# Kernel tuning notes

Measured on AMD Instinct MI355X. Metric: run time of the kernel, lower is better.

The kernel has to match this reference:

```python
import jax, jax.numpy as jnp
import numpy as np

B, L, D, H, DFF = 4, 2048, 1024, 16, 4096
DH = D // H
INF = 1e12


def setup_inputs() -> dict:
    key = jax.random.key(0)
    ks = jax.random.split(key, 20)
    s = lambda fan_in: 1.0 / np.sqrt(fan_in)
    inp = {
        'x': jax.random.normal(ks[0], (B, L, D), jnp.float32),
        'mask': jax.random.bernoulli(ks[1], 0.1, (B, 1, 1, L)),
        'wq': jax.random.normal(ks[2], (D, D), jnp.float32) * s(D),
        'bq': jnp.zeros((D,), jnp.float32),
        'wk': jax.random.normal(ks[3], (D, D), jnp.float32) * s(D),
        'bk': jnp.zeros((D,), jnp.float32),
        'wv': jax.random.normal(ks[4], (D, D), jnp.float32) * s(D),
        'bv': jnp.zeros((D,), jnp.float32),
        'wo': jax.random.normal(ks[5], (D, D), jnp.float32) * s(D),
        'bo': jnp.zeros((D,), jnp.float32),
        'w1': jax.random.normal(ks[6], (D, DFF), jnp.float32) * s(D),
        'b1': jnp.zeros((DFF,), jnp.float32),
        'w2': jax.random.normal(ks[7], (DFF, D), jnp.float32) * s(DFF),
        'b2': jnp.zeros((D,), jnp.float32),
        'g1': jnp.ones((D,), jnp.float32),
        'beta1': jnp.zeros((D,), jnp.float32),
        'g2': jnp.ones((D,), jnp.float32),
        'beta2': jnp.zeros((D,), jnp.float32),
    }
    return inp


def _layernorm(x, g, b, eps=1e-5):
    mu = jnp.mean(x, axis=-1, keepdims=True)
    var = jnp.mean(jnp.square(x - mu), axis=-1, keepdims=True)
    return (x - mu) * jax.lax.rsqrt(var + eps) * g + b


def reference(x, mask, wq, bq, wk, bk, wv, bv, wo, bo, w1, b1, w2, b2, g1, beta1, g2, beta2):
    # --- self attention ---
    def split_heads(t):  # [B,L,D] -> [B,H,L,DH]
        return t.reshape(B, L, H, DH).transpose(0, 2, 1, 3)

    Q = split_heads(x @ wq + bq)
    K = split_heads(x @ wk + bk)
    V = split_heads(x @ wv + bv)

    dots = jnp.einsum('bhqd,bhkd->bhqk', Q, K) / np.sqrt(DH)  # [B,H,L,L]
    dots = jnp.where(mask, -INF, dots)
    attn = jax.nn.softmax(dots, axis=-1)
    out = jnp.einsum('bhqk,bhkd->bhqd', attn, V)
    out = out.transpose(0, 2, 1, 3).reshape(B, L, D)
    out = out @ wo + bo

    x = _layernorm(x + out, g1, beta1)

    # --- feed forward ---
    h = jax.nn.relu(x @ w1 + b1)
    ff = h @ w2 + b2
    x = _layernorm(x + ff, g2, beta2)
    return x
```

## Files before the change

kernel.cpp:

```cpp
#include <hip/hip_runtime.h>
#include <hip/hip_bf16.h>

#define B_   4
#define L_   2048
#define D_   1024
#define H_   16
#define DH_  64
#define DFF_ 4096
#define M_   (B_ * L_)

typedef __attribute__((ext_vector_type(8))) short bf16x8;
typedef __attribute__((ext_vector_type(4))) float f32x4;

#define GLOAD16(gp, lp)                                                       \
  __builtin_amdgcn_global_load_lds(                                           \
      (const __attribute__((address_space(1))) unsigned int*)(gp),            \
      (__attribute__((address_space(3))) unsigned int*)(lp), 16, 0, 0)

#if __has_builtin(__builtin_amdgcn_exp2f)
#define EXP2F(x) __builtin_amdgcn_exp2f(x)
#else
#define EXP2F(x) exp2f(x)
#endif

__device__ __forceinline__ float bf2f(unsigned short u) {
  return __uint_as_float(((unsigned)u) << 16);
}

__global__ void prep_all(const float4* __restrict__ x4,
                         ushort4* __restrict__ xb4,
                         const unsigned int* __restrict__ mraw,
                         float* __restrict__ maskf,
                         const float* __restrict__ bq,
                         const float* __restrict__ bk,
                         const float* __restrict__ bv,
                         float* __restrict__ biasc) {
  const int id = blockIdx.x;
  if (id < 8192) {
    const int i = id * 256 + threadIdx.x;
    float4 v = x4[i];
    __hip_bfloat16 a = __float2bfloat16(v.x);
    __hip_bfloat16 b = __float2bfloat16(v.y);
    __hip_bfloat16 c = __float2bfloat16(v.z);
    __hip_bfloat16 d = __float2bfloat16(v.w);
    ushort4 o;
    o.x = *reinterpret_cast<unsigned short*>(&a);
    o.y = *reinterpret_cast<unsigned short*>(&b);
    o.z = *reinterpret_cast<unsigned short*>(&c);
    o.w = *reinterpret_cast<unsigned short*>(&d);
    xb4[i] = o;
    return;
  }
  __shared__ int flags[2];
  if (threadIdx.x < 2) flags[threadIdx.x] = 0;
  __syncthreads();
  int nf32 = 0, n01 = 0;
  for (int i = threadIdx.x; i < 2048; i += 256) {
    unsigned w = mraw[i];
    if (w != 0u && w != 0x3f800000u) nf32 = 1;
    if (w > 1u) n01 = 1;
  }
  if (nf32) atomicOr(&flags[0], 1);
  if (n01)  atomicOr(&flags[1], 1);
  __syncthreads();
  const int mode = (!flags[0]) ? 0 : ((!flags[1]) ? 1 : 2);
  const int mi = (id - 8192) * 256 + threadIdx.x;
  if (mi < B_ * L_) {
    bool mk;
    if (mode == 0)      mk = reinterpret_cast<const float*>(mraw)[mi] != 0.f;
    else if (mode == 1) mk = reinterpret_cast<const int*>(mraw)[mi] != 0;
    else                mk = reinterpret_cast<const unsigned char*>(mraw)[mi] != 0;
    maskf[mi] = mk ? -1e12f : -32.0f;
  }
  if (id == 8192) {
#pragma unroll
    for (int j = 0; j < 4; ++j) {
      const int c = j * 256 + threadIdx.x;
      biasc[c] = bq[c];
      biasc[D_ + c] = bk[c];
      biasc[2 * D_ + c] = bv[c];
    }
  }
}

__global__ void transpose_cvt_all(
    const float* __restrict__ wq, const float* __restrict__ wk,
    const float* __restrict__ wv, const float* __restrict__ wo,
    const float* __restrict__ w1, const float* __restrict__ w2,
    __hip_bfloat16* __restrict__ WQT, __hip_bfloat16* __restrict__ WKT,
    __hip_bfloat16* __restrict__ WVT, __hip_bfloat16* __restrict__ WOT,
    __hip_bfloat16* __restrict__ W1T, __hip_bfloat16* __restrict__ W2T) {
  __shared__ float t[32][33];
  const int id = blockIdx.x;
  const float* W;
  __hip_bfloat16* Wt;
  int K, N, rem;
  if (id < 4096) {
    const int which = id >> 10;
    W  = which == 0 ? wq : which == 1 ? wk : which == 2 ? wv : wo;
    Wt = which == 0 ? WQT : which == 1 ? WKT : which == 2 ? WVT : WOT;
    K = D_; N = D_; rem = id & 1023;
  } else if (id < 8192) {
    W = w1; Wt = W1T; K = D_; N = DFF_; rem = id - 4096;
  } else {
    W = w2; Wt = W2T; K = DFF_; N = D_; rem = id - 8192;
  }
  const int ntx = N >> 5;
  const int n0 = (rem % ntx) * 32, k0 = (rem / ntx) * 32;
  const int tx = threadIdx.x, ty = threadIdx.y;
#pragma unroll
  for (int i = 0; i < 4; ++i)
    t[ty + i * 8][tx] = W[(size_t)(k0 + ty + i * 8) * N + n0 + tx];
  __syncthreads();
#pragma unroll
  for (int i = 0; i < 4; ++i)
    Wt[(size_t)(n0 + ty + i * 8) * K + k0 + tx] =
        __float2bfloat16(t[tx][ty + i * 8]);
}

__global__ void transpose_v(const __hip_bfloat16* __restrict__ Vin,
                            __hip_bfloat16* __restrict__ Vt) {
  __shared__ __hip_bfloat16 t[32][33];
  const int l0 = blockIdx.x * 32, d0 = blockIdx.y * 32, b = blockIdx.z;
  const int tx = threadIdx.x, ty = threadIdx.y;
#pragma unroll
  for (int i = 0; i < 4; ++i)
    t[ty + i * 8][tx] = Vin[(size_t)(b * L_ + l0 + ty + i * 8) * D_ + d0 + tx];
  __syncthreads();
#pragma unroll
  for (int i = 0; i < 4; ++i) {
    int d = d0 + ty + i * 8;
    Vt[(size_t)(b * D_ + d) * L_ + l0 + tx] = t[tx][ty + i * 8];
  }
}

#define STAGE8(matptr, stride, ldsbase, tile, kh, rowbase)                    \
  {                                                                           \
    _Pragma("unroll")                                                         \
    for (int j_ = 0; j_ < 2; ++j_) {                                          \
      const int s_ = j_ * 512 + tid;                                          \
      const int row_ = s_ >> 2;                                               \
      const int q_ = (s_ & 3) ^ ((row_ >> 1) & 3);                            \
      GLOAD16(&matptr[(size_t)((rowbase) + row_) * (stride) + (tile) * 64 +   \
                      (kh) * 32 + q_ * 8],                                    \
              (ldsbase) + (j_ * 512 + (w << 6)) * 16);                        \
    }                                                                         \
  }

#define PHASE8(bufoff, rh, ks, dovm, ...)                                     \
  {                                                                           \
    if ((rh) == 0) {                                                          \
      _Pragma("unroll")                                                       \
      for (int j = 0; j < 4; ++j) {                                           \
        const int br = wn * 64 + j * 16 + r16;                                \
        bfr[j] = *reinterpret_cast<const bf16x8*>(                            \
            ldsB + (bufoff) + (ks) * 16384 + br * 64 +                        \
            ((hi * 16) ^ (((br >> 1) & 3) << 4)));                            \
      }                                                                       \
    }                                                                         \
    bf16x8 af[4];                                                             \
    _Pragma("unroll")                                                         \
    for (int i = 0; i < 4; ++i) {                                             \
      const int ar = wm * 128 + (rh) * 64 + i * 16 + r16;                     \
      af[i] = *reinterpret_cast<const bf16x8*>(                               \
          ldsA + (bufoff) + (ks) * 16384 + ar * 64 +                          \
          ((hi * 16) ^ (((ar >> 1) & 3) << 4)));                              \
    }                                                                         \
    __VA_ARGS__;                                                              \
    __builtin_amdgcn_s_barrier();                                             \
    asm volatile("s_waitcnt lgkmcnt(0)" ::: "memory");                        \
    __builtin_amdgcn_sched_barrier(0);                                        \
    __builtin_amdgcn_s_setprio(1);                                            \
    _Pragma("unroll")                                                         \
    for (int i = 0; i < 4; ++i)                                               \
      _Pragma("unroll")                                                       \
      for (int j = 0; j < 4; ++j)                                             \
        acc[(rh) * 4 + i][j] = __builtin_amdgcn_mfma_f32_16x16x32_bf16(       \
            af[i], bfr[j], acc[(rh) * 4 + i][j], 0, 0, 0);                    \
    __builtin_amdgcn_s_setprio(0);                                            \
    if (dovm) {                                                               \
      asm volatile("s_waitcnt vmcnt(4)" ::: "memory");                        \
      __builtin_amdgcn_sched_barrier(0);                                      \
    }                                                                         \
    __builtin_amdgcn_s_barrier();                                             \
  }

template <int EP>
__global__ __launch_bounds__(512, 1) void gemm8(
    const __hip_bfloat16* __restrict__ A, const __hip_bfloat16* __restrict__ Bt,
    const float* __restrict__ bias, void* __restrict__ out,
    int M, int N, int K, int lda, int ldb) {
  __shared__ __align__(16) char lds8[131072];
  char* const ldsA = lds8;
  char* const ldsB = lds8 + 65536;

  const int tid = threadIdx.x;
  const int lane = tid & 63;
  const int w = tid >> 6;
  const int wm = w >> 2;
  const int wn = w & 3;
  const int r16 = lane & 15;
  const int hi = lane >> 4;

  const int nwg = gridDim.x;
  const int orig = blockIdx.x;
  const int swz = (orig & 7) * (nwg >> 3) + (orig >> 3);

  int bm, bn, kh = 0;
  const __hip_bfloat16* Ap = A;
  const __hip_bfloat16* Bp = Bt;
  if (EP == 4) {
    kh = swz & 1;
    const int rest = swz >> 1;
    bm = (rest & 31) * 256;
    bn = (rest >> 5) * 256;
    Ap += (size_t)kh * K;
    Bp += (size_t)kh * K;
  } else {
    bm = (swz & 31) * 256;
    bn = (swz >> 5) * 256;
  }

  f32x4 acc[8][4];
#pragma unroll
  for (int i = 0; i < 8; ++i)
#pragma unroll
    for (int j = 0; j < 4; ++j) acc[i][j] = (f32x4){0.f, 0.f, 0.f, 0.f};
  bf16x8 bfr[4];

  const int nkt = K >> 6;
  const int nit = nkt >> 1;

  STAGE8(Ap, lda, ldsA, 0, 0, bm);
  STAGE8(Bp, ldb, ldsB, 0, 0, bn);
  STAGE8(Ap, lda, ldsA + 16384, 0, 1, bm);
  STAGE8(Bp, ldb, ldsB + 16384, 0, 1, bn);
  STAGE8(Ap, lda, ldsA + 32768, 1, 0, bm);
  STAGE8(Bp, ldb, ldsB + 32768, 1, 0, bn);
  asm volatile("s_waitcnt vmcnt(4)" ::: "memory");
  __builtin_amdgcn_sched_barrier(0);
  __builtin_amdgcn_s_barrier();

  for (int it = 0; it < nit; ++it) {
    const int kt = it * 2;
    const bool hn = (it + 1) < nit;
    PHASE8(0, 0, 0, 0, STAGE8(Ap, lda, ldsA + 49152, kt + 1, 1, bm));
    PHASE8(0, 1, 0, 0, STAGE8(Bp, ldb, ldsB + 49152, kt + 1, 1, bn));
    PHASE8(0, 0, 1, 0, if (hn) STAGE8(Ap, lda, ldsA, kt + 2, 0, bm));
    PHASE8(0, 1, 1, 1, if (hn) STAGE8(Bp, ldb, ldsB, kt + 2, 0, bn));
    PHASE8(32768, 0, 0, 0, if (hn) STAGE8(Ap, lda, ldsA + 16384, kt + 2, 1, bm));
    PHASE8(32768, 1, 0, 0, if (hn) STAGE8(Bp, ldb, ldsB + 16384, kt + 2, 1, bn));
    PHASE8(32768, 0, 1, 0, if (hn) STAGE8(Ap, lda, ldsA + 32768, kt + 3, 0, bm));
    PHASE8(32768, 1, 1, 1, if (hn) STAGE8(Bp, ldb, ldsB + 32768, kt + 3, 0, bn));
  }

#pragma unroll
  for (int ri = 0; ri < 8; ++ri) {
#pragma unroll
    for (int j = 0; j < 4; ++j) {
      const int col = bn + wn * 64 + j * 16 + r16;
      const float bv = (EP == 4) ? 0.f : bias[col];
#pragma unroll
      for (int r = 0; r < 4; ++r) {
        const int row = bm + wm * 128 + ri * 16 + hi * 4 + r;
        const float v = acc[ri][j][r] + bv;
        if (EP == 1) {
          ((__hip_bfloat16*)out)[(size_t)row * N + col] =
              __float2bfloat16(v > 0.f ? v : 0.f);
        } else if (EP == 3) {
          __hip_bfloat16* outp =
              (__hip_bfloat16*)out + (size_t)(col >> 10) * (M_ * D_);
          outp[(size_t)row * 1024 + (col & 1023)] = __float2bfloat16(v);
        } else {
          __hip_bfloat16* outp =
              (__hip_bfloat16*)out + (size_t)kh * ((size_t)M * N);
          outp[(size_t)row * N + col] = __float2bfloat16(v);
        }
      }
    }
  }
}

template <int EP>
__global__ __launch_bounds__(256) void gemm_bt(
    const __hip_bfloat16* __restrict__ A, const __hip_bfloat16* __restrict__ Bt,
    const float* __restrict__ bias, const float* __restrict__ res,
    void* __restrict__ out, int M, int N, int K) {
  __shared__ __align__(16) char As[128 * 64];
  __shared__ __align__(16) char Bs[128 * 64];
  const int tid = threadIdx.x;
  const int lane = tid & 63;
  const int w = tid >> 6;
  const int wm = w >> 1, wn = w & 1;
  const int bm = blockIdx.x * 128;
  const int bn = blockIdx.y * 128;
  const int r16 = lane & 15;
  const int hi = lane >> 4;

  f32x4 acc[4][4];
#pragma unroll
  for (int m = 0; m < 4; ++m)
#pragma unroll
    for (int n = 0; n < 4; ++n) acc[m][n] = (f32x4){0.f, 0.f, 0.f, 0.f};

  for (int k0 = 0; k0 < K; k0 += 32) {
    __syncthreads();
#pragma unroll
    for (int c = 0; c < 2; ++c) {
      const int seg = c * 256 + tid;
      const int row = seg >> 2;
      const int csl = (seg & 3) ^ (row & 3);
      GLOAD16(&A[(size_t)(bm + row) * K + k0 + csl * 8],
              As + (c * 256 + w * 64) * 16);
      GLOAD16(&Bt[(size_t)(bn + row) * K + k0 + csl * 8],
              Bs + (c * 256 + w * 64) * 16);
    }
    __syncthreads();

    bf16x8 af[4], bfr[4];
#pragma unroll
    for (int m = 0; m < 4; ++m) {
      const int arow = wm * 64 + m * 16 + r16;
      af[m] = *reinterpret_cast<const bf16x8*>(
          As + arow * 64 + ((hi * 16) ^ ((arow & 3) << 4)));
    }
#pragma unroll
    for (int n = 0; n < 4; ++n) {
      const int brow = wn * 64 + n * 16 + r16;
      bfr[n] = *reinterpret_cast<const bf16x8*>(
          Bs + brow * 64 + ((hi * 16) ^ ((brow & 3) << 4)));
    }
#pragma unroll
    for (int m = 0; m < 4; ++m)
#pragma unroll
      for (int n = 0; n < 4; ++n)
        acc[m][n] = __builtin_amdgcn_mfma_f32_16x16x32_bf16(af[m], bfr[n],
                                                            acc[m][n], 0, 0, 0);
  }

  const int rg = hi * 4;
#pragma unroll
  for (int m = 0; m < 4; ++m) {
#pragma unroll
    for (int n = 0; n < 4; ++n) {
      const int col = bn + wn * 64 + n * 16 + r16;
      const float bv = bias[col];
#pragma unroll
      for (int r = 0; r < 4; ++r) {
        const int row = bm + wm * 64 + m * 16 + rg + r;
        const size_t idx = (size_t)row * N + col;
        float v = acc[m][n][r] + bv;
        if (EP == 0) {
          ((__hip_bfloat16*)out)[idx] = __float2bfloat16(v);
        } else {
          ((float*)out)[idx] = v + res[idx];
        }
      }
    }
  }
}

__global__ __launch_bounds__(256) void attn_kernel(
    const __hip_bfloat16* __restrict__ Qg, const __hip_bfloat16* __restrict__ Kg,
    const __hip_bfloat16* __restrict__ VTg,
    const float* __restrict__ maskf,
    __hip_bfloat16* __restrict__ Og) {
  __shared__ __align__(16) char Kl[64 * 128];
  __shared__ __align__(16) char Vl[64 * 128];
  __shared__ __align__(16) char Pl[4][32 * 128];
  __shared__ float maskb[64];

  const int tid = threadIdx.x;
  const int lane = tid & 63;
  const int w = tid >> 6;
  const int hi = lane >> 4;
  const int r16 = lane & 15;
  const int swzk = (r16 & 7) << 4;

  const int nwg = gridDim.x;
  const int orig = blockIdx.x;
  const int swb = (orig & 7) * (nwg >> 3) + (orig >> 3);
  const int qb = swb & 15;
  const int bh = swb >> 4;
  const int b = bh >> 4;
  const int h = bh & 15;
  const int qbase = qb * 128 + w * 32;

  const float C = 0.18033688011112042f;

  bf16x8 qf[2][2];
#pragma unroll
  for (int m = 0; m < 2; ++m)
#pragma unroll
    for (int ks = 0; ks < 2; ++ks)
      qf[m][ks] = *reinterpret_cast<const bf16x8*>(
          &Qg[(size_t)(b * L_ + qbase + m * 16 + r16) * D_ + h * DH_ +
              ks * 32 + hi * 8]);

  float lrun[2] = {0.f, 0.f};
  f32x4 o[2][4];
#pragma unroll
  for (int m = 0; m < 2; ++m)
#pragma unroll
    for (int nd = 0; nd < 4; ++nd) o[m][nd] = (f32x4){0.f, 0.f, 0.f, 0.f};

  char* const Plw = Pl[w];

  for (int kv0 = 0; kv0 < L_; kv0 += 64) {
    __syncthreads();
#pragma unroll
    for (int c = 0; c < 2; ++c) {
      const int seg = c * 256 + tid;
      const int row = seg >> 3;
      const int csl = (seg & 7) ^ (row & 7);
      GLOAD16(&Kg[(size_t)(b * L_ + kv0 + row) * D_ + h * DH_ + csl * 8],
              Kl + (c * 256 + w * 64) * 16);
      GLOAD16(&VTg[(size_t)(b * D_ + h * DH_ + row) * L_ + kv0 + csl * 8],
              Vl + (c * 256 + w * 64) * 16);
    }
    if (tid < 64) maskb[tid] = maskf[(size_t)b * L_ + kv0 + tid];
    __syncthreads();

    f32x4 sacc[2][4];
#pragma unroll
    for (int m = 0; m < 2; ++m)
#pragma unroll
      for (int n = 0; n < 4; ++n) sacc[m][n] = (f32x4){0.f, 0.f, 0.f, 0.f};
    __builtin_amdgcn_s_setprio(1);
#pragma unroll
    for (int n = 0; n < 4; ++n) {
      const int krow = n * 16 + r16;
#pragma unroll
      for (int ks = 0; ks < 2; ++ks) {
        const bf16x8 kf = *reinterpret_cast<const bf16x8*>(
            Kl + krow * 128 + ((ks * 64 + hi * 16) ^ swzk));
#pragma unroll
        for (int m = 0; m < 2; ++m)
          sacc[m][n] = __builtin_amdgcn_mfma_f32_16x16x32_bf16(
              kf, qf[m][ks], sacc[m][n], 0, 0, 0);
      }
    }
    __builtin_amdgcn_s_setprio(0);

#pragma unroll
    for (int m = 0; m < 2; ++m) {
      float ls = 0.f;
      const int prow = m * 16 + r16;
#pragma unroll
      for (int n = 0; n < 4; ++n) {
        const float4 mv =
            *reinterpret_cast<const float4*>(&maskb[n * 16 + hi * 4]);
        const float e0 = EXP2F(fmaf(sacc[m][n][0], C, mv.x));
        const float e1 = EXP2F(fmaf(sacc[m][n][1], C, mv.y));
        const float e2 = EXP2F(fmaf(sacc[m][n][2], C, mv.z));
        const float e3 = EXP2F(fmaf(sacc[m][n][3], C, mv.w));
        ls += (e0 + e1) + (e2 + e3);
        union { unsigned long long u; unsigned short us[4]; } pk;
        __hip_bfloat16 t0 = __float2bfloat16(e0);
        __hip_bfloat16 t1 = __float2bfloat16(e1);
        __hip_bfloat16 t2 = __float2bfloat16(e2);
        __hip_bfloat16 t3 = __float2bfloat16(e3);
        pk.us[0] = *reinterpret_cast<unsigned short*>(&t0);
        pk.us[1] = *reinterpret_cast<unsigned short*>(&t1);
        pk.us[2] = *reinterpret_cast<unsigned short*>(&t2);
        pk.us[3] = *reinterpret_cast<unsigned short*>(&t3);
        *reinterpret_cast<unsigned long long*>(
            Plw + prow * 128 + ((n * 32 + hi * 8) ^ swzk)) = pk.u;
      }
      lrun[m] += ls;
    }

    bf16x8 pa[2][2];
#pragma unroll
    for (int m = 0; m < 2; ++m)
#pragma unroll
      for (int ks = 0; ks < 2; ++ks)
        pa[m][ks] = *reinterpret_cast<const bf16x8*>(
            Plw + (m * 16 + r16) * 128 + ((ks * 64 + hi * 16) ^ swzk));
    __builtin_amdgcn_s_setprio(1);
#pragma unroll
    for (int nd = 0; nd < 4; ++nd) {
      const int vrow = nd * 16 + r16;
#pragma unroll
      for (int ks = 0; ks < 2; ++ks) {
        const bf16x8 vb = *reinterpret_cast<const bf16x8*>(
            Vl + vrow * 128 + ((ks * 64 + hi * 16) ^ swzk));
#pragma unroll
        for (int m = 0; m < 2; ++m)
          o[m][nd] = __builtin_amdgcn_mfma_f32_16x16x32_bf16(pa[m][ks], vb,
                                                             o[m][nd], 0, 0, 0);
      }
    }
    __builtin_amdgcn_s_setprio(0);
  }

#pragma unroll
  for (int m = 0; m < 2; ++m) {
    lrun[m] += __shfl_xor(lrun[m], 16, 64);
    lrun[m] += __shfl_xor(lrun[m], 32, 64);
    const float inv = 1.f / lrun[m];
    float invr[4];
#pragma unroll
    for (int r = 0; r < 4; ++r)
      invr[r] = __shfl(inv, (lane & 48) | (hi * 4 + r), 64);
#pragma unroll
    for (int r = 0; r < 4; ++r) {
      const int q = qbase + m * 16 + hi * 4 + r;
#pragma unroll
      for (int nd = 0; nd < 4; ++nd)
        Og[(size_t)(b * L_ + q) * D_ + h * DH_ + nd * 16 + r16] =
            __float2bfloat16(o[m][nd][r] * invr[r]);
    }
  }
}

__global__ __launch_bounds__(256) void layernorm_kernel(
    const float* __restrict__ in, const float* __restrict__ g,
    const float* __restrict__ be, float* __restrict__ outf,
    __hip_bfloat16* __restrict__ outb) {
  const int row = blockIdx.x;
  const int tid = threadIdx.x;
  const float4 v = reinterpret_cast<const float4*>(in + (size_t)row * D_)[tid];
  float s = v.x + v.y + v.z + v.w;
  float ss = v.x * v.x + v.y * v.y + v.z * v.z + v.w * v.w;
#pragma unroll
  for (int off = 1; off < 64; off <<= 1) {
    s += __shfl_xor(s, off, 64);
    ss += __shfl_xor(ss, off, 64);
  }
  __shared__ float red[8];
  const int w = tid >> 6, lane = tid & 63;
  if (lane == 0) { red[w] = s; red[4 + w] = ss; }
  __syncthreads();
  s = red[0] + red[1] + red[2] + red[3];
  ss = red[4] + red[5] + red[6] + red[7];
  const float mu = s * (1.f / D_);
  const float rs = rsqrtf(ss * (1.f / D_) - mu * mu + 1e-5f);
  const float4 gv = reinterpret_cast<const float4*>(g)[tid];
  const float4 bv = reinterpret_cast<const float4*>(be)[tid];
  float4 ov;
  ov.x = (v.x - mu) * rs * gv.x + bv.x;
  ov.y = (v.y - mu) * rs * gv.y + bv.y;
  ov.z = (v.z - mu) * rs * gv.z + bv.z;
  ov.w = (v.w - mu) * rs * gv.w + bv.w;
  reinterpret_cast<float4*>(outf + (size_t)row * D_)[tid] = ov;
  if (outb) {
    __hip_bfloat16 t[4] = {__float2bfloat16(ov.x), __float2bfloat16(ov.y),
                           __float2bfloat16(ov.z), __float2bfloat16(ov.w)};
    *reinterpret_cast<uint2*>(&outb[(size_t)row * D_ + tid * 4]) =
        *reinterpret_cast<const uint2*>(t);
  }
}

__global__ __launch_bounds__(256) void ln_addres(
    const __hip_bfloat16* __restrict__ OP, const float* __restrict__ x,
    const float* __restrict__ g, const float* __restrict__ be,
    float* __restrict__ outf, __hip_bfloat16* __restrict__ outb) {
  const int row = blockIdx.x;
  const int tid = threadIdx.x;
  const ushort4 a4 = reinterpret_cast<const ushort4*>(OP + (size_t)row * D_)[tid];
  const float4 xr = reinterpret_cast<const float4*>(x + (size_t)row * D_)[tid];
  float4 v;
  v.x = bf2f(a4.x) + xr.x;
  v.y = bf2f(a4.y) + xr.y;
  v.z = bf2f(a4.z) + xr.z;
  v.w = bf2f(a4.w) + xr.w;
  float s = v.x + v.y + v.z + v.w;
  float ss = v.x * v.x + v.y * v.y + v.z * v.z + v.w * v.w;
#pragma unroll
  for (int off = 1; off < 64; off <<= 1) {
    s += __shfl_xor(s, off, 64);
    ss += __shfl_xor(ss, off, 64);
  }
  __shared__ float red[8];
  const int w = tid >> 6, lane = tid & 63;
  if (lane == 0) { red[w] = s; red[4 + w] = ss; }
  __syncthreads();
  s = red[0] + red[1] + red[2] + red[3];
  ss = red[4] + red[5] + red[6] + red[7];
  const float mu = s * (1.f / D_);
  const float rs = rsqrtf(ss * (1.f / D_) - mu * mu + 1e-5f);
  const float4 gv = reinterpret_cast<const float4*>(g)[tid];
  const float4 bv = reinterpret_cast<const float4*>(be)[tid];
  float4 ov;
  ov.x = (v.x - mu) * rs * gv.x + bv.x;
  ov.y = (v.y - mu) * rs * gv.y + bv.y;
  ov.z = (v.z - mu) * rs * gv.z + bv.z;
  ov.w = (v.w - mu) * rs * gv.w + bv.w;
  reinterpret_cast<float4*>(outf + (size_t)row * D_)[tid] = ov;
  __hip_bfloat16 t[4] = {__float2bfloat16(ov.x), __float2bfloat16(ov.y),
                         __float2bfloat16(ov.z), __float2bfloat16(ov.w)};
  *reinterpret_cast<uint2*>(&outb[(size_t)row * D_ + tid * 4]) =
      *reinterpret_cast<const uint2*>(t);
}

__global__ __launch_bounds__(256) void combine_ln2(
    const __hip_bfloat16* __restrict__ P0, const __hip_bfloat16* __restrict__ P1,
    const float* __restrict__ res, const float* __restrict__ b2,
    const float* __restrict__ g, const float* __restrict__ be,
    float* __restrict__ out) {
  const int row = blockIdx.x;
  const int tid = threadIdx.x;
  const ushort4 a4 =
      reinterpret_cast<const ushort4*>(P0 + (size_t)row * D_)[tid];
  const ushort4 b4 =
      reinterpret_cast<const ushort4*>(P1 + (size_t)row * D_)[tid];
  const float4 rr = reinterpret_cast<const float4*>(res + (size_t)row * D_)[tid];
  const float4 bb = reinterpret_cast<const float4*>(b2)[tid];
  float4 v;
  v.x = bf2f(a4.x) + bf2f(b4.x) + rr.x + bb.x;
  v.y = bf2f(a4.y) + bf2f(b4.y) + rr.y + bb.y;
  v.z = bf2f(a4.z) + bf2f(b4.z) + rr.z + bb.z;
  v.w = bf2f(a4.w) + bf2f(b4.w) + rr.w + bb.w;
  float s = v.x + v.y + v.z + v.w;
  float ss = v.x * v.x + v.y * v.y + v.z * v.z + v.w * v.w;
#pragma unroll
  for (int off = 1; off < 64; off <<= 1) {
    s += __shfl_xor(s, off, 64);
    ss += __shfl_xor(ss, off, 64);
  }
  __shared__ float red[8];
  const int w = tid >> 6, lane = tid & 63;
  if (lane == 0) { red[w] = s; red[4 + w] = ss; }
  __syncthreads();
  s = red[0] + red[1] + red[2] + red[3];
  ss = red[4] + red[5] + red[6] + red[7];
  const float mu = s * (1.f / D_);
  const float rs = rsqrtf(ss * (1.f / D_) - mu * mu + 1e-5f);
  const float4 gv = reinterpret_cast<const float4*>(g)[tid];
  const float4 bv = reinterpret_cast<const float4*>(be)[tid];
  float4 ov;
  ov.x = (v.x - mu) * rs * gv.x + bv.x;
  ov.y = (v.y - mu) * rs * gv.y + bv.y;
  ov.z = (v.z - mu) * rs * gv.z + bv.z;
  ov.w = (v.w - mu) * rs * gv.w + bv.w;
  reinterpret_cast<float4*>(out + (size_t)row * D_)[tid] = ov;
}

extern "C" void kernel_launch(void* const* d_in, const int* in_sizes, int n_in,
                              void* d_out, int out_size, void* d_ws,
                              size_t ws_size, hipStream_t stream) {
  (void)in_sizes; (void)n_in; (void)out_size;
  const float* x   = (const float*)d_in[0];
  const void*  msk = d_in[1];
  const float* wq  = (const float*)d_in[2];
  const float* bq  = (const float*)d_in[3];
  const float* wk  = (const float*)d_in[4];
  const float* bk  = (const float*)d_in[5];
  const float* wv  = (const float*)d_in[6];
  const float* bv  = (const float*)d_in[7];
  const float* wo  = (const float*)d_in[8];
  const float* bo  = (const float*)d_in[9];
  const float* w1  = (const float*)d_in[10];
  const float* b1  = (const float*)d_in[11];
  const float* w2  = (const float*)d_in[12];
  const float* b2  = (const float*)d_in[13];
  const float* g1  = (const float*)d_in[14];
  const float* be1 = (const float*)d_in[15];
  const float* g2  = (const float*)d_in[16];
  const float* be2 = (const float*)d_in[17];

  char* ws = (char*)d_ws;
  float*          MASKF = (float*)(ws + 256);
  float*          BIASC = (float*)(ws + 40960);
  __hip_bfloat16* XB    = (__hip_bfloat16*)(ws + 65536);
  __hip_bfloat16* WQT   = (__hip_bfloat16*)(ws + 16842752);
  __hip_bfloat16* WKT   = (__hip_bfloat16*)(ws + 18939904);
  __hip_bfloat16* WVT   = (__hip_bfloat16*)(ws + 21037056);
  __hip_bfloat16* WOT   = (__hip_bfloat16*)(ws + 23134208);
  __hip_bfloat16* W1T   = (__hip_bfloat16*)(ws + 25231360);
  __hip_bfloat16* W2T   = (__hip_bfloat16*)(ws + 33619968);
  __hip_bfloat16* QB    = (__hip_bfloat16*)(ws + 42008576);
  __hip_bfloat16* KB    = (__hip_bfloat16*)(ws + 58785792);
  __hip_bfloat16* VB    = (__hip_bfloat16*)(ws + 75563008);
  __hip_bfloat16* OB    = (__hip_bfloat16*)(ws + 92340224);
  __hip_bfloat16* HB    = QB;
  __hip_bfloat16* VT    = (__hip_bfloat16*)(ws + 109117440);
  __hip_bfloat16* OP    = VT;
  float*          R1    = (float*)(ws + 125894656);
  __hip_bfloat16* P0    = (__hip_bfloat16*)(ws + 159449088);
  __hip_bfloat16* P1    = (__hip_bfloat16*)(ws + 176226304);
  float*          OUT   = (float*)d_out;
  const bool use_splitk = ws_size >= 193003520ull;

  prep_all<<<8224, 256, 0, stream>>>((const float4*)x, (ushort4*)XB,
                                     (const unsigned int*)msk, MASKF,
                                     bq, bk, bv, BIASC);
  transpose_cvt_all<<<12288, dim3(32, 8), 0, stream>>>(
      wq, wk, wv, wo, w1, w2, WQT, WKT, WVT, WOT, W1T, W2T);

  gemm8<3><<<dim3((M_ / 256) * (3 * D_ / 256)), 512, 0, stream>>>(
      XB, WQT, BIASC, QB, M_, 3 * D_, D_, D_, D_);

  transpose_v<<<dim3(L_ / 32, D_ / 32, B_), dim3(32, 8), 0, stream>>>(VB, VT);
  attn_kernel<<<dim3(B_ * H_ * (L_ / 128)), 256, 0, stream>>>(QB, KB, VT, MASKF, OB);

  gemm_bt<0><<<dim3(M_ / 128, D_ / 128), 256, 0, stream>>>(OB, WOT, bo, nullptr, OP, M_, D_, D_);
  ln_addres<<<M_, 256, 0, stream>>>(OP, x, g1, be1, R1, XB);

  gemm8<1><<<dim3((M_ / 256) * (DFF_ / 256)), 512, 0, stream>>>(
      XB, W1T, b1, HB, M_, DFF_, D_, D_, D_);
  if (use_splitk) {
    gemm8<4><<<dim3((M_ / 256) * (D_ / 256) * 2), 512, 0, stream>>>(
        HB, W2T, nullptr, P0, M_, D_, DFF_ / 2, DFF_, DFF_);
    combine_ln2<<<M_, 256, 0, stream>>>(P0, P1, R1, b2, g2, be2, OUT);
  } else {
    gemm_bt<2><<<dim3(M_ / 128, D_ / 128), 256, 0, stream>>>(HB, W2T, b2, R1, OUT, M_, D_, DFF_);
    layernorm_kernel<<<M_, 256, 0, stream>>>(OUT, g2, be2, OUT, nullptr);
  }
}
```

Measured before the change: 433.3 us.

## Compute softmax denominator via MFMA and use split-K gemm8 for output projection

In attention, the per-row sum of exponentials is now taken with an extra MFMA against a ones vector, using the same bf16-rounded probabilities as the PV product. This replaces scalar adds and the cross-lane shuffles at the end. The mask values are loaded once per KV tile instead of once per m iteration. The output projection also switches from gemm_bt to the 256-tile gemm8 split-K path, and the two partials plus bias are combined inside a new fused residual+layernorm kernel. This costs extra MFMA work and bf16 partial traffic, and the denominator is now built from rounded values.

After: 416.8 us. 1.04x faster.

```diff
diff --git a/kernel.cpp b/kernel.cpp
--- a/kernel.cpp
+++ b/kernel.cpp
@@ -387,6 +387,8 @@
   const int qbase = qb * 128 + w * 32;
 
   const float C = 0.18033688011112042f;
+  const short ob = (short)0x3f80;
+  const bf16x8 vone = {ob, ob, ob, ob, ob, ob, ob, ob};
 
   bf16x8 qf[2][2];
 #pragma unroll
@@ -397,12 +399,14 @@
           &Qg[(size_t)(b * L_ + qbase + m * 16 + r16) * D_ + h * DH_ +
               ks * 32 + hi * 8]);
 
-  float lrun[2] = {0.f, 0.f};
   f32x4 o[2][4];
-#pragma unroll
-  for (int m = 0; m < 2; ++m)
+  f32x4 oden[2];
+#pragma unroll
+  for (int m = 0; m < 2; ++m) {
+    oden[m] = (f32x4){0.f, 0.f, 0.f, 0.f};
 #pragma unroll
     for (int nd = 0; nd < 4; ++nd) o[m][nd] = (f32x4){0.f, 0.f, 0.f, 0.f};
+  }
 
   char* const Plw = Pl[w];
 
@@ -442,19 +446,19 @@
     }
     __builtin_amdgcn_s_setprio(0);
 
+    float4 mv[4];
+#pragma unroll
+    for (int n = 0; n < 4; ++n)
+      mv[n] = *reinterpret_cast<const float4*>(&maskb[n * 16 + hi * 4]);
 #pragma unroll
     for (int m = 0; m < 2; ++m) {
-      float ls = 0.f;
       const int prow = m * 16 + r16;
 #pragma unroll
       for (int n = 0; n < 4; ++n) {
-        const float4 mv =
-            *reinterpret_cast<const float4*>(&maskb[n * 16 + hi * 4]);
-        const float e0 = EXP2F(fmaf(sacc[m][n][0], C, mv.x));
-        const float e1 = EXP2F(fmaf(sacc[m][n][1], C, mv.y));
-        const float e2 = EXP2F(fmaf(sacc[m][n][2], C, mv.z));
-        const float e3 = EXP2F(fmaf(sacc[m][n][3], C, mv.w));
-        ls += (e0 + e1) + (e2 + e3);
+        const float e0 = EXP2F(fmaf(sacc[m][n][0], C, mv[n].x));
+        const float e1 = EXP2F(fmaf(sacc[m][n][1], C, mv[n].y));
+        const float e2 = EXP2F(fmaf(sacc[m][n][2], C, mv[n].z));
+        const float e3 = EXP2F(fmaf(sacc[m][n][3], C, mv[n].w));
         union { unsigned long long u; unsigned short us[4]; } pk;
         __hip_bfloat16 t0 = __float2bfloat16(e0);
         __hip_bfloat16 t1 = __float2bfloat16(e1);
@@ -467,7 +471,6 @@
         *reinterpret_cast<unsigned long long*>(
             Plw + prow * 128 + ((n * 32 + hi * 8) ^ swzk)) = pk.u;
       }
-      lrun[m] += ls;
     }
 
     bf16x8 pa[2][2];
@@ -479,6 +482,12 @@
             Plw + (m * 16 + r16) * 128 + ((ks * 64 + hi * 16) ^ swzk));
     __builtin_amdgcn_s_setprio(1);
 #pragma unroll
+    for (int m = 0; m < 2; ++m)
+#pragma unroll
+      for (int ks = 0; ks < 2; ++ks)
+        oden[m] = __builtin_amdgcn_mfma_f32_16x16x32_bf16(pa[m][ks], vone,
+                                                          oden[m], 0, 0, 0);
+#pragma unroll
     for (int nd = 0; nd < 4; ++nd) {
       const int vrow = nd * 16 + r16;
 #pragma unroll
@@ -496,20 +505,14 @@
 
 #pragma unroll
   for (int m = 0; m < 2; ++m) {
-    lrun[m] += __shfl_xor(lrun[m], 16, 64);
-    lrun[m] += __shfl_xor(lrun[m], 32, 64);
-    const float inv = 1.f / lrun[m];
-    float invr[4];
-#pragma unroll
-    for (int r = 0; r < 4; ++r)
-      invr[r] = __shfl(inv, (lane & 48) | (hi * 4 + r), 64);
 #pragma unroll
     for (int r = 0; r < 4; ++r) {
+      const float ir = 1.f / oden[m][r];
       const int q = qbase + m * 16 + hi * 4 + r;
 #pragma unroll
       for (int nd = 0; nd < 4; ++nd)
         Og[(size_t)(b * L_ + q) * D_ + h * DH_ + nd * 16 + r16] =
-            __float2bfloat16(o[m][nd][r] * invr[r]);
+            __float2bfloat16(o[m][nd][r] * ir);
     }
   }
 }
@@ -565,6 +568,51 @@
   v.y = bf2f(a4.y) + xr.y;
   v.z = bf2f(a4.z) + xr.z;
   v.w = bf2f(a4.w) + xr.w;
+  float s = v.x + v.y + v.z + v.w;
+  float ss = v.x * v.x + v.y * v.y + v.z * v.z + v.w * v.w;
+#pragma unroll
+  for (int off = 1; off < 64; off <<= 1) {
+    s += __shfl_xor(s, off, 64);
+    ss += __shfl_xor(ss, off, 64);
+  }
+  __shared__ float red[8];
+  const int w = tid >> 6, lane = tid & 63;
+  if (lane == 0) { red[w] = s; red[4 + w] = ss; }
+  __syncthreads();
+  s = red[0] + red[1] + red[2] + red[3];
+  ss = red[4] + red[5] + red[6] + red[7];
+  const float mu = s * (1.f / D_);
+  const float rs = rsqrtf(ss * (1.f / D_) - mu * mu + 1e-5f);
+  const float4 gv = reinterpret_cast<const float4*>(g)[tid];
+  const float4 bv = reinterpret_cast<const float4*>(be)[tid];
+  float4 ov;
+  ov.x = (v.x - mu) * rs * gv.x + bv.x;
+  ov.y = (v.y - mu) * rs * gv.y + bv.y;
+  ov.z = (v.z - mu) * rs * gv.z + bv.z;
+  ov.w = (v.w - mu) * rs * gv.w + bv.w;
+  reinterpret_cast<float4*>(outf + (size_t)row * D_)[tid] = ov;
+  __hip_bfloat16 t[4] = {__float2bfloat16(ov.x), __float2bfloat16(ov.y),
+                         __float2bfloat16(ov.z), __float2bfloat16(ov.w)};
+  *reinterpret_cast<uint2*>(&outb[(size_t)row * D_ + tid * 4]) =
+      *reinterpret_cast<const uint2*>(t);
+}
+
+__global__ __launch_bounds__(256) void ln_addres_sk(
+    const __hip_bfloat16* __restrict__ P0, const __hip_bfloat16* __restrict__ P1,
+    const float* __restrict__ x, const float* __restrict__ bo,
+    const float* __restrict__ g, const float* __restrict__ be,
+    float* __restrict__ outf, __hip_bfloat16* __restrict__ outb) {
+  const int row = blockIdx.x;
+  const int tid = threadIdx.x;
+  const ushort4 a4 = reinterpret_cast<const ushort4*>(P0 + (size_t)row * D_)[tid];
+  const ushort4 b4 = reinterpret_cast<const ushort4*>(P1 + (size_t)row * D_)[tid];
+  const float4 xr = reinterpret_cast<const float4*>(x + (size_t)row * D_)[tid];
+  const float4 bb = reinterpret_cast<const float4*>(bo)[tid];
+  float4 v;
+  v.x = bf2f(a4.x) + bf2f(b4.x) + xr.x + bb.x;
+  v.y = bf2f(a4.y) + bf2f(b4.y) + xr.y + bb.y;
+  v.z = bf2f(a4.z) + bf2f(b4.z) + xr.z + bb.z;
+  v.w = bf2f(a4.w) + bf2f(b4.w) + xr.w + bb.w;
   float s = v.x + v.y + v.z + v.w;
   float ss = v.x * v.x + v.y * v.y + v.z * v.z + v.w * v.w;
 #pragma unroll
@@ -695,8 +743,14 @@
   transpose_v<<<dim3(L_ / 32, D_ / 32, B_), dim3(32, 8), 0, stream>>>(VB, VT);
   attn_kernel<<<dim3(B_ * H_ * (L_ / 128)), 256, 0, stream>>>(QB, KB, VT, MASKF, OB);
 
-  gemm_bt<0><<<dim3(M_ / 128, D_ / 128), 256, 0, stream>>>(OB, WOT, bo, nullptr, OP, M_, D_, D_);
-  ln_addres<<<M_, 256, 0, stream>>>(OP, x, g1, be1, R1, XB);
+  if (use_splitk) {
+    gemm8<4><<<dim3((M_ / 256) * (D_ / 256) * 2), 512, 0, stream>>>(
+        OB, WOT, nullptr, P0, M_, D_, D_ / 2, D_, D_);
+    ln_addres_sk<<<M_, 256, 0, stream>>>(P0, P1, x, bo, g1, be1, R1, XB);
+  } else {
+    gemm_bt<0><<<dim3(M_ / 128, D_ / 128), 256, 0, stream>>>(OB, WOT, bo, nullptr, OP, M_, D_, D_);
+    ln_addres<<<M_, 256, 0, stream>>>(OP, x, g1, be1, R1, XB);
+  }
 
   gemm8<1><<<dim3((M_ / 256) * (DFF_ / 256)), 512, 0, stream>>>(
       XB, W1T, b1, HB, M_, DFF_, D_, D_, D_);
```
